# Kernel tuning notes

Measured on AMD Instinct MI355X. Metric: run time of the kernel, lower is better.

## Reference

```python
import jax, jax.numpy as jnp
import numpy as np

EPS = 1e-12  # torch F.normalize eps


def setup_inputs() -> dict:
    key = jax.random.key(0)
    k1, k2, k3 = jax.random.split(key, 3)
    b, c, n, h, w = 8, 64, 8, 64, 64
    dims = 32
    x = jax.random.normal(k1, (b, c, n, h, w), dtype=jnp.float32)
    # 1x1 conv kernels collapse to [out_ch, in_ch] matrices
    w_q = jax.random.normal(k2, (dims, c), dtype=jnp.float32) * (1.0 / np.sqrt(c))
    w_kv = jax.random.normal(k3, (2 * dims, c), dtype=jnp.float32) * (1.0 / np.sqrt(c))
    return {"x": x, "w_q": w_q, "w_kv": w_kv}


def _l2norm(t, axis):
    nrm = jnp.sqrt(jnp.sum(t * t, axis=axis, keepdims=True))
    return t / jnp.maximum(nrm, EPS)


def reference(x, w_q, w_kv):
    b, c, n, h, w = x.shape
    d = w_q.shape[0]
    # spa_q: 1x1 stride-1 conv == channel GEMM -> [b, d, n, h, w]
    q = jnp.einsum('bcnhw,dc->bdnhw', x, w_q)
    x_s = x[:, :, :, ::2, ::2]                       # [b, c, n, h2, w2]
    kv = jnp.einsum('bcnhw,ec->benhw', x_s, w_kv)    # [b, 2d, n, h2, w2]
    k, v = kv[:, :d], kv[:, d:]
    h2, w2 = k.shape[-2], k.shape[-1]
    # unfold_q: b (h w) (d n)
    uq = q.transpose(0, 3, 4, 1, 2).reshape(b, h * w, d * n)
    # unfold_k: b (d n) (h2 w2)
    uk = k.reshape(b, d * n, h2 * w2)
    # unfold_v: b (h2 w2) (d n)
    uv = v.transpose(0, 3, 4, 1, 2).reshape(b, h2 * w2, d * n)
    uq = _l2norm(uq, axis=-1)
    uk = _l2norm(uk, axis=-2)
    att = jax.nn.softmax(jnp.einsum('bqf,bfk->bqk', uq, uk), axis=-1)
    out = jnp.einsum('bqk,bkf->bqf', att, uv)        # [b, h*w, d*n]
    # b (h w) (d n) -> b d n h w
    return out.reshape(b, h, w, d, n).transpose(0, 3, 4, 1, 2)
```

## Files before the change

### kernel.cpp

```cpp
#include <hip/hip_runtime.h>


typedef __attribute__((ext_vector_type(8))) short short8;
typedef __attribute__((ext_vector_type(4))) float floatx4;
typedef __attribute__((ext_vector_type(2))) unsigned uintx2;

__device__ __forceinline__ short f2bf(float f) {
    unsigned u = __builtin_bit_cast(unsigned, f);
    u += 0x7fffu + ((u >> 16) & 1u);
    return (short)(u >> 16);
}

__device__ __forceinline__ unsigned cvtpk_bf16(float lo, float hi) {
    unsigned r;
    asm("v_cvt_pk_bf16_f32 %0, %1, %2" : "=v"(r) : "v"(lo), "v"(hi));
    return r;
}

__global__ __launch_bounds__(256) void proj(const float* __restrict__ x,
                                            const float* __restrict__ wq,
                                            const float* __restrict__ wkv,
                                            short* __restrict__ qraw,
                                            short* __restrict__ kraw,
                                            short* __restrict__ vraw) {
    int b = blockIdx.x >> 6, y = blockIdx.x & 63;
    int t = threadIdx.x;
    int n = t >> 5, dg = (t >> 3) & 3, xc = t & 7;
    bool kv = (y & 1) == 0;
    int y2 = y >> 1;

    __shared__ __align__(16) float wq_s[64 * 32];
    __shared__ __align__(16) float wkv_s[64 * 64];
    __shared__ __align__(16) float xs[128 * 36];
    __shared__ __align__(16) short k_lds[16 * 264];
    __shared__ __align__(16) short v_lds[256 * 16];
    __shared__ float red[32 * 33];
    __shared__ float nrm[32];
    short* q_lds = (short*)xs;

    for (int i = t; i < 2048; i += 256) { int d = i >> 6, c = i & 63; wq_s[c * 32 + d] = wq[i]; }
    for (int i = t; i < 4096; i += 256) { int e = i >> 6, c = i & 63; wkv_s[c * 64 + e] = wkv[i]; }
    const float* xb = x + (size_t)b * 2097152 + y * 64;

    for (int xh = 0; xh < 2; ++xh) {
        float qa[8][4], ka[8][2], va[8][2];
#pragma unroll
        for (int j = 0; j < 8; ++j) {
            qa[j][0] = qa[j][1] = qa[j][2] = qa[j][3] = 0.f;
            ka[j][0] = ka[j][1] = 0.f; va[j][0] = va[j][1] = 0.f;
        }
        for (int cc = 0; cc < 4; ++cc) {
            __syncthreads();
#pragma unroll
            for (int it = 0; it < 4; ++it) {
                int i = it * 256 + t, cn = i >> 3, e = i & 7;
                float4 v = *(const float4*)(xb + (size_t)(cc * 16 + (cn >> 3)) * 32768 + (cn & 7) * 4096 + xh * 32 + e * 4);
                *(float4*)(xs + cn * 36 + e * 4) = v;
            }
            __syncthreads();
            for (int c = 0; c < 16; ++c) {
                float4 xv = *(const float4*)(xs + (c * 8 + n) * 36 + xc * 4);
                float xw[4] = {xv.x, xv.y, xv.z, xv.w};
                int cg = cc * 16 + c;
                float4 wqa = *(const float4*)(wq_s + cg * 32 + dg * 8);
                float4 wqb = *(const float4*)(wq_s + cg * 32 + dg * 8 + 4);
                float wj[8] = {wqa.x, wqa.y, wqa.z, wqa.w, wqb.x, wqb.y, wqb.z, wqb.w};
#pragma unroll
                for (int j = 0; j < 8; ++j)
#pragma unroll
                    for (int i2 = 0; i2 < 4; ++i2) qa[j][i2] += wj[j] * xw[i2];
                if (kv) {
                    float4 wka = *(const float4*)(wkv_s + cg * 64 + dg * 8);
                    float4 wkb = *(const float4*)(wkv_s + cg * 64 + dg * 8 + 4);
                    float4 wva = *(const float4*)(wkv_s + cg * 64 + 32 + dg * 8);
                    float4 wvb = *(const float4*)(wkv_s + cg * 64 + 32 + dg * 8 + 4);
                    float wk[8] = {wka.x, wka.y, wka.z, wka.w, wkb.x, wkb.y, wkb.z, wkb.w};
                    float wv2[8] = {wva.x, wva.y, wva.z, wva.w, wvb.x, wvb.y, wvb.z, wvb.w};
#pragma unroll
                    for (int j = 0; j < 8; ++j) {
                        ka[j][0] += wk[j] * xw[0]; ka[j][1] += wk[j] * xw[2];
                        va[j][0] += wv2[j] * xw[0]; va[j][1] += wv2[j] * xw[2];
                    }
                }
            }
        }
        __syncthreads();
#pragma unroll
        for (int i2 = 0; i2 < 4; ++i2) {
            float s = 0.f;
#pragma unroll
            for (int j = 0; j < 8; ++j) s += qa[j][i2] * qa[j][i2];
            red[(xc * 4 + i2) * 33 + n * 4 + dg] = s;
        }
        __syncthreads();
        if (t < 32) {
            float s = 0.f;
            for (int k = 0; k < 32; ++k) s += red[t * 33 + k];
            nrm[t] = 1.f / fmaxf(sqrtf(s), 1e-12f);
        }
        __syncthreads();
#pragma unroll
        for (int i2 = 0; i2 < 4; ++i2) {
            float sc = nrm[xc * 4 + i2];
#pragma unroll
            for (int j = 0; j < 8; ++j)
                q_lds[(xc * 4 + i2) * 264 + (dg * 8 + j) * 8 + n] = f2bf(qa[j][i2] * sc);
        }
        __syncthreads();
        {
            size_t qg = ((size_t)b * 4096 + y * 64 + xh * 32) * 256;
#pragma unroll
            for (int it = 0; it < 4; ++it) {
                int r = it * 8 + (t >> 5), sg = t & 31;
                *(uint4*)(qraw + qg + (size_t)r * 256 + sg * 8) = *(const uint4*)(q_lds + r * 264 + sg * 8);
            }
        }
        if (kv) {
            __syncthreads();
#pragma unroll
            for (int ii = 0; ii < 2; ++ii) {
                float s = 0.f;
#pragma unroll
                for (int j = 0; j < 8; ++j) s += ka[j][ii] * ka[j][ii];
                red[(xc * 2 + ii) * 33 + n * 4 + dg] = s;
            }
            __syncthreads();
            if (t < 16) {
                float s = 0.f;
                for (int k = 0; k < 32; ++k) s += red[t * 33 + k];
                nrm[t] = 1.f / fmaxf(sqrtf(s), 1e-12f);
            }
            __syncthreads();
#pragma unroll
            for (int ii = 0; ii < 2; ++ii) {
                float sc = nrm[xc * 2 + ii];
#pragma unroll
                for (int j = 0; j < 8; ++j) {
                    int f = (dg * 8 + j) * 8 + n;
                    k_lds[(xc * 2 + ii) * 264 + f] = f2bf(ka[j][ii] * sc);
                    v_lds[f * 16 + xc * 2 + ii] = f2bf(va[j][ii]);
                }
            }
            __syncthreads();
            size_t kg = ((size_t)b * 1024 + y2 * 32 + xh * 16) * 256;
#pragma unroll
            for (int it = 0; it < 2; ++it) {
                int r = it * 8 + (t >> 5), sg = t & 31;
                *(uint4*)(kraw + kg + (size_t)r * 256 + sg * 8) = *(const uint4*)(k_lds + r * 264 + sg * 8);
            }
            size_t vg = (size_t)b * 262144 + (size_t)y2 * 32 + xh * 16;
#pragma unroll
            for (int it = 0; it < 2; ++it) {
                int idx = it * 256 + t, f = idx >> 1, hh = idx & 1;
                *(uint4*)(vraw + vg + (size_t)f * 1024 + hh * 8) = *(const uint4*)(v_lds + f * 16 + hh * 8);
            }
        }
    }
}

__global__ __launch_bounds__(512, 2) void attn(const short* __restrict__ qraw,
                                               const short* __restrict__ kraw,
                                               const short* __restrict__ vraw,
                                               float* __restrict__ out) {
    int b = blockIdx.x >> 5, qt = blockIdx.x & 31;
    int t = threadIdx.x, wv = t >> 6, lane = t & 63, l16 = lane & 15, quad = lane >> 4;

    __shared__ __align__(16) short k_s[2][32 * 264];
    __shared__ __align__(16) short v_s[2][256 * 40];
    __shared__ __align__(16) short p_s[2][128 * 40];
    __shared__ float dsum[2][128];

    int kt = wv & 1, pp = wv >> 1;
    int fh = wv & 3, ph = wv >> 2;

    short8 qf[2][8];
    const short* qb = qraw + ((size_t)b * 4096 + qt * 128 + pp * 32) * 256;
#pragma unroll
    for (int pt = 0; pt < 2; ++pt)
#pragma unroll
        for (int fs = 0; fs < 8; ++fs)
            qf[pt][fs] = *(const short8*)(qb + (pt * 16 + l16) * 256 + fs * 32 + quad * 8);

    floatx4 acc[4][4];
#pragma unroll
    for (int i = 0; i < 4; ++i)
#pragma unroll
        for (int j = 0; j < 4; ++j) acc[i][j] = (floatx4){0.f, 0.f, 0.f, 0.f};
    float dacc0 = 0.f, dacc1 = 0.f;

    int krow = t >> 4, kseg = t & 15;
    int vrow = t >> 1, vhalf = t & 1;
    int sk = (kseg >> 2) & 1, sv = (t >> 4) & 1;
    const short* kbase = kraw + ((size_t)b * 1024 + krow) * 256 + kseg * 16;
    const short* vbase = vraw + ((size_t)b * 256 + vrow) * 1024 + vhalf * 16;

    short8 kst[2], vst[2];
#pragma unroll
    for (int j = 0; j < 2; ++j) {
        kst[j] = *(const short8*)(kbase + j * 8);
        vst[j] = *(const short8*)(vbase + j * 8);
    }
#pragma unroll
    for (int j = 0; j < 2; ++j) {
        *(short8*)(k_s[0] + krow * 264 + kseg * 16 + (j ^ sk) * 8) = kst[j];
        *(short8*)(v_s[0] + vrow * 40 + vhalf * 16 + (j ^ sv) * 8) = vst[j];
    }
#pragma unroll
    for (int j = 0; j < 2; ++j) {
        kst[j] = *(const short8*)(kbase + 8192 + j * 8);
        vst[j] = *(const short8*)(vbase + 32 + j * 8);
    }
    __syncthreads();

    int s2 = (l16 >> 3) & 1;
    for (int kc = 0; kc < 32; ++kc) {
        int cur = kc & 1, nxt = cur ^ 1;
        floatx4 cc0 = (floatx4){0.f, 0.f, 0.f, 0.f};
        floatx4 cc1 = (floatx4){0.f, 0.f, 0.f, 0.f};
        const short* krd = k_s[cur] + (kt * 16 + l16) * 264;
        __builtin_amdgcn_s_setprio(1);
#pragma unroll
        for (int fs = 0; fs < 8; ++fs) {
            short8 a = *(const short8*)(krd + fs * 32 + (quad ^ ((fs >> 1) & 1)) * 8);
            cc0 = __builtin_amdgcn_mfma_f32_16x16x32_bf16(a, qf[0][fs], cc0, 0, 0, 0);
            cc1 = __builtin_amdgcn_mfma_f32_16x16x32_bf16(a, qf[1][fs], cc1, 0, 0, 0);
        }
        __builtin_amdgcn_s_setprio(0);
        {
            float e0 = __expf(cc0[0]), e1 = __expf(cc0[1]);
            float e2 = __expf(cc0[2]), e3 = __expf(cc0[3]);
            dacc0 += (e0 + e1) + (e2 + e3);
            uintx2 w0; w0[0] = cvtpk_bf16(e0, e1); w0[1] = cvtpk_bf16(e2, e3);
            *(uintx2*)(p_s[cur] + (pp * 32 + l16) * 40 + kt * 16 + quad * 4) = w0;
            float f0 = __expf(cc1[0]), f1 = __expf(cc1[1]);
            float f2 = __expf(cc1[2]), f3 = __expf(cc1[3]);
            dacc1 += (f0 + f1) + (f2 + f3);
            uintx2 w1; w1[0] = cvtpk_bf16(f0, f1); w1[1] = cvtpk_bf16(f2, f3);
            *(uintx2*)(p_s[cur] + (pp * 32 + 16 + l16) * 40 + kt * 16 + quad * 4) = w1;
        }
        __syncthreads();

        if (kc < 31) {
#pragma unroll
            for (int j = 0; j < 2; ++j) {
                *(short8*)(k_s[nxt] + krow * 264 + kseg * 16 + (j ^ sk) * 8) = kst[j];
                *(short8*)(v_s[nxt] + vrow * 40 + vhalf * 16 + (j ^ sv) * 8) = vst[j];
            }
        }
        short8 av[4];
#pragma unroll
        for (int fl = 0; fl < 4; ++fl)
            av[fl] = *(const short8*)(v_s[cur] + (fh * 64 + fl * 16 + l16) * 40 + (quad ^ s2) * 8);
        __builtin_amdgcn_s_setprio(1);
#pragma unroll
        for (int p2 = 0; p2 < 4; ++p2) {
            short8 bq = *(const short8*)(p_s[cur] + (ph * 64 + p2 * 16 + l16) * 40 + quad * 8);
#pragma unroll
            for (int fl = 0; fl < 4; ++fl)
                acc[p2][fl] = __builtin_amdgcn_mfma_f32_16x16x32_bf16(av[fl], bq, acc[p2][fl], 0, 0, 0);
        }
        __builtin_amdgcn_s_setprio(0);
        if (kc < 30) {
            int koff = (kc + 2) * 8192, voff = (kc + 2) * 32;
#pragma unroll
            for (int j = 0; j < 2; ++j) {
                kst[j] = *(const short8*)(kbase + koff + j * 8);
                vst[j] = *(const short8*)(vbase + voff + j * 8);
            }
        }
        __syncthreads();
    }
    dacc0 += __shfl_xor(dacc0, 16); dacc0 += __shfl_xor(dacc0, 32);
    dacc1 += __shfl_xor(dacc1, 16); dacc1 += __shfl_xor(dacc1, 32);
    if (quad == 0) {
        dsum[kt][pp * 32 + l16] = dacc0;
        dsum[kt][pp * 32 + 16 + l16] = dacc1;
    }
    __syncthreads();
    float* ob = out + (size_t)b * 1048576 + qt * 128;
#pragma unroll
    for (int p2 = 0; p2 < 4; ++p2) {
        int pcol = ph * 64 + p2 * 16 + l16;
        float inv = 1.f / (dsum[0][pcol] + dsum[1][pcol]);
#pragma unroll
        for (int fl = 0; fl < 4; ++fl) {
            int f0 = fh * 64 + fl * 16 + quad * 4;
#pragma unroll
            for (int r = 0; r < 4; ++r)
                ob[(size_t)(f0 + r) * 4096 + pcol] = acc[p2][fl][r] * inv;
        }
    }
}

extern "C" void kernel_launch(void* const* d_in, const int* in_sizes, int n_in,
                              void* d_out, int out_size, void* d_ws, size_t ws_size,
                              hipStream_t stream) {
    (void)in_sizes; (void)n_in; (void)out_size; (void)ws_size;
    const float* x   = (const float*)d_in[0];
    const float* wqp = (const float*)d_in[1];
    const float* wkv = (const float*)d_in[2];
    float* out = (float*)d_out;

    char* ws = (char*)d_ws;
    short* qraw = (short*)ws;
    short* kraw = (short*)(ws + 16777216);
    short* vraw = (short*)(ws + 16777216 + 4194304);

    proj<<<512, 256, 0, stream>>>(x, wqp, wkv, qraw, kraw, vraw);
    attn<<<256, 512, 0, stream>>>(qraw, kraw, vraw, out);
}
```

Baseline: 184.0 us.

## Process both x-halves in parallel with 512-thread proj blocks and swizzled LDS stores

```diff
diff --git a/kernel.cpp b/kernel.cpp
--- a/kernel.cpp
+++ b/kernel.cpp
@@ -17,80 +17,114 @@
     return r;
 }
 
-__global__ __launch_bounds__(256) void proj(const float* __restrict__ x,
-                                            const float* __restrict__ wq,
-                                            const float* __restrict__ wkv,
-                                            short* __restrict__ qraw,
-                                            short* __restrict__ kraw,
-                                            short* __restrict__ vraw) {
+__global__ __launch_bounds__(512, 4) void proj(const float* __restrict__ x,
+                                               const float* __restrict__ wq,
+                                               const float* __restrict__ wkv,
+                                               short* __restrict__ qraw,
+                                               short* __restrict__ kraw,
+                                               short* __restrict__ vraw) {
     int b = blockIdx.x >> 6, y = blockIdx.x & 63;
     int t = threadIdx.x;
-    int n = t >> 5, dg = (t >> 3) & 3, xc = t & 7;
+    int th = t & 255, xh = t >> 8;
+    int n = th >> 5, dg = (th >> 3) & 3, xc = th & 7;
     bool kv = (y & 1) == 0;
     int y2 = y >> 1;
 
     __shared__ __align__(16) float wq_s[64 * 32];
     __shared__ __align__(16) float wkv_s[64 * 64];
-    __shared__ __align__(16) float xs[128 * 36];
-    __shared__ __align__(16) short k_lds[16 * 264];
-    __shared__ __align__(16) short v_lds[256 * 16];
-    __shared__ float red[32 * 33];
-    __shared__ float nrm[32];
-    short* q_lds = (short*)xs;
-
-    for (int i = t; i < 2048; i += 256) { int d = i >> 6, c = i & 63; wq_s[c * 32 + d] = wq[i]; }
-    for (int i = t; i < 4096; i += 256) { int e = i >> 6, c = i & 63; wkv_s[c * 64 + e] = wkv[i]; }
+    __shared__ __align__(16) char region[37376];
+    __shared__ float red[64 * 33];
+    __shared__ float nrm[64];
+    float* xs    = (float*)region;
+    short* q_lds = (short*)region;
+    short* k_lds = (short*)region;
+    short* v_lds = (short*)(region + 16896);
+
+    for (int i = t; i < 2048; i += 512) { int d = i >> 6, c = i & 63; wq_s[c * 32 + d] = wq[i]; }
+    for (int i = t; i < 4096; i += 512) { int e = i >> 6, c = i & 63; wkv_s[c * 64 + e] = wkv[i]; }
     const float* xb = x + (size_t)b * 2097152 + y * 64;
 
-    for (int xh = 0; xh < 2; ++xh) {
-        float qa[8][4], ka[8][2], va[8][2];
-#pragma unroll
-        for (int j = 0; j < 8; ++j) {
-            qa[j][0] = qa[j][1] = qa[j][2] = qa[j][3] = 0.f;
-            ka[j][0] = ka[j][1] = 0.f; va[j][0] = va[j][1] = 0.f;
-        }
-        for (int cc = 0; cc < 4; ++cc) {
-            __syncthreads();
-#pragma unroll
-            for (int it = 0; it < 4; ++it) {
-                int i = it * 256 + t, cn = i >> 3, e = i & 7;
-                float4 v = *(const float4*)(xb + (size_t)(cc * 16 + (cn >> 3)) * 32768 + (cn & 7) * 4096 + xh * 32 + e * 4);
-                *(float4*)(xs + cn * 36 + e * 4) = v;
-            }
-            __syncthreads();
-            for (int c = 0; c < 16; ++c) {
-                float4 xv = *(const float4*)(xs + (c * 8 + n) * 36 + xc * 4);
-                float xw[4] = {xv.x, xv.y, xv.z, xv.w};
-                int cg = cc * 16 + c;
-                float4 wqa = *(const float4*)(wq_s + cg * 32 + dg * 8);
-                float4 wqb = *(const float4*)(wq_s + cg * 32 + dg * 8 + 4);
-                float wj[8] = {wqa.x, wqa.y, wqa.z, wqa.w, wqb.x, wqb.y, wqb.z, wqb.w};
-#pragma unroll
-                for (int j = 0; j < 8; ++j)
-#pragma unroll
-                    for (int i2 = 0; i2 < 4; ++i2) qa[j][i2] += wj[j] * xw[i2];
-                if (kv) {
-                    float4 wka = *(const float4*)(wkv_s + cg * 64 + dg * 8);
-                    float4 wkb = *(const float4*)(wkv_s + cg * 64 + dg * 8 + 4);
-                    float4 wva = *(const float4*)(wkv_s + cg * 64 + 32 + dg * 8);
-                    float4 wvb = *(const float4*)(wkv_s + cg * 64 + 32 + dg * 8 + 4);
-                    float wk[8] = {wka.x, wka.y, wka.z, wka.w, wkb.x, wkb.y, wkb.z, wkb.w};
-                    float wv2[8] = {wva.x, wva.y, wva.z, wva.w, wvb.x, wvb.y, wvb.z, wvb.w};
-#pragma unroll
-                    for (int j = 0; j < 8; ++j) {
-                        ka[j][0] += wk[j] * xw[0]; ka[j][1] += wk[j] * xw[2];
-                        va[j][0] += wv2[j] * xw[0]; va[j][1] += wv2[j] * xw[2];
-                    }
+    float qa[8][4], ka[8][2], va[8][2];
+#pragma unroll
+    for (int j = 0; j < 8; ++j) {
+        qa[j][0] = qa[j][1] = qa[j][2] = qa[j][3] = 0.f;
+        ka[j][0] = ka[j][1] = 0.f; va[j][0] = va[j][1] = 0.f;
+    }
+    for (int cc = 0; cc < 4; ++cc) {
+        __syncthreads();
+#pragma unroll
+        for (int it = 0; it < 4; ++it) {
+            int i = it * 512 + t, cn = i >> 4, e = i & 15;
+            float4 v = *(const float4*)(xb + (size_t)(cc * 16 + (cn >> 3)) * 32768 + (cn & 7) * 4096 + e * 4);
+            *(float4*)(xs + cn * 72 + e * 4) = v;
+        }
+        __syncthreads();
+        for (int c = 0; c < 16; ++c) {
+            float4 xv = *(const float4*)(xs + (c * 8 + n) * 72 + xh * 32 + xc * 4);
+            float xw[4] = {xv.x, xv.y, xv.z, xv.w};
+            int cg = cc * 16 + c;
+            float4 wqa = *(const float4*)(wq_s + cg * 32 + dg * 8);
+            float4 wqb = *(const float4*)(wq_s + cg * 32 + dg * 8 + 4);
+            float wj[8] = {wqa.x, wqa.y, wqa.z, wqa.w, wqb.x, wqb.y, wqb.z, wqb.w};
+#pragma unroll
+            for (int j = 0; j < 8; ++j)
+#pragma unroll
+                for (int i2 = 0; i2 < 4; ++i2) qa[j][i2] += wj[j] * xw[i2];
+            if (kv) {
+                float4 wka = *(const float4*)(wkv_s + cg * 64 + dg * 8);
+                float4 wkb = *(const float4*)(wkv_s + cg * 64 + dg * 8 + 4);
+                float4 wva = *(const float4*)(wkv_s + cg * 64 + 32 + dg * 8);
+                float4 wvb = *(const float4*)(wkv_s + cg * 64 + 32 + dg * 8 + 4);
+                float wk[8] = {wka.x, wka.y, wka.z, wka.w, wkb.x, wkb.y, wkb.z, wkb.w};
+                float wv2[8] = {wva.x, wva.y, wva.z, wva.w, wvb.x, wvb.y, wvb.z, wvb.w};
+#pragma unroll
+                for (int j = 0; j < 8; ++j) {
+                    ka[j][0] += wk[j] * xw[0]; ka[j][1] += wk[j] * xw[2];
+                    va[j][0] += wv2[j] * xw[0]; va[j][1] += wv2[j] * xw[2];
                 }
             }
         }
-        __syncthreads();
-#pragma unroll
-        for (int i2 = 0; i2 < 4; ++i2) {
+    }
+#pragma unroll
+    for (int i2 = 0; i2 < 4; ++i2) {
+        float s = 0.f;
+#pragma unroll
+        for (int j = 0; j < 8; ++j) s += qa[j][i2] * qa[j][i2];
+        red[(xh * 32 + xc * 4 + i2) * 33 + n * 4 + dg] = s;
+    }
+    __syncthreads();
+    if (t < 64) {
+        float s = 0.f;
+        for (int k = 0; k < 32; ++k) s += red[t * 33 + k];
+        nrm[t] = 1.f / fmaxf(sqrtf(s), 1e-12f);
+    }
+    __syncthreads();
+#pragma unroll
+    for (int i2 = 0; i2 < 4; ++i2) {
+        int row = xh * 32 + xc * 4 + i2;
+        float sc = nrm[row];
+#pragma unroll
+        for (int j = 0; j < 8; ++j)
+            q_lds[row * 264 + (dg * 8 + (j ^ dg)) * 8 + n] = f2bf(qa[j][i2] * sc);
+    }
+    __syncthreads();
+    {
+        size_t qg = ((size_t)b * 4096 + y * 64) * 256;
+#pragma unroll
+        for (int it = 0; it < 4; ++it) {
+            int idx = it * 512 + t, r = idx >> 5, sg = idx & 31;
+            *(uint4*)(qraw + qg + (size_t)r * 256 + sg * 8) =
+                *(const uint4*)(q_lds + r * 264 + (sg ^ ((sg >> 3) & 3)) * 8);
+        }
+    }
+    if (kv) {
+        __syncthreads();
+#pragma unroll
+        for (int ii = 0; ii < 2; ++ii) {
             float s = 0.f;
 #pragma unroll
-            for (int j = 0; j < 8; ++j) s += qa[j][i2] * qa[j][i2];
-            red[(xc * 4 + i2) * 33 + n * 4 + dg] = s;
+            for (int j = 0; j < 8; ++j) s += ka[j][ii] * ka[j][ii];
+            red[(xh * 16 + xc * 2 + ii) * 33 + n * 4 + dg] = s;
         }
         __syncthreads();
         if (t < 32) {
@@ -100,60 +134,28 @@
         }
         __syncthreads();
 #pragma unroll
-        for (int i2 = 0; i2 < 4; ++i2) {
-            float sc = nrm[xc * 4 + i2];
-#pragma unroll
-            for (int j = 0; j < 8; ++j)
-                q_lds[(xc * 4 + i2) * 264 + (dg * 8 + j) * 8 + n] = f2bf(qa[j][i2] * sc);
-        }
-        __syncthreads();
-        {
-            size_t qg = ((size_t)b * 4096 + y * 64 + xh * 32) * 256;
-#pragma unroll
-            for (int it = 0; it < 4; ++it) {
-                int r = it * 8 + (t >> 5), sg = t & 31;
-                *(uint4*)(qraw + qg + (size_t)r * 256 + sg * 8) = *(const uint4*)(q_lds + r * 264 + sg * 8);
+        for (int ii = 0; ii < 2; ++ii) {
+            int row = xh * 16 + xc * 2 + ii;
+            float sc = nrm[row];
+#pragma unroll
+            for (int j = 0; j < 8; ++j) {
+                k_lds[row * 264 + (dg * 8 + (j ^ dg)) * 8 + n] = f2bf(ka[j][ii] * sc);
+                v_lds[(dg * 64 + j * 8 + n) * 40 + row] = f2bf(va[j][ii]);
             }
         }
-        if (kv) {
-            __syncthreads();
-#pragma unroll
-            for (int ii = 0; ii < 2; ++ii) {
-                float s = 0.f;
-#pragma unroll
-                for (int j = 0; j < 8; ++j) s += ka[j][ii] * ka[j][ii];
-                red[(xc * 2 + ii) * 33 + n * 4 + dg] = s;
-            }
-            __syncthreads();
-            if (t < 16) {
-                float s = 0.f;
-                for (int k = 0; k < 32; ++k) s += red[t * 33 + k];
-                nrm[t] = 1.f / fmaxf(sqrtf(s), 1e-12f);
-            }
-            __syncthreads();
-#pragma unroll
-            for (int ii = 0; ii < 2; ++ii) {
-                float sc = nrm[xc * 2 + ii];
-#pragma unroll
-                for (int j = 0; j < 8; ++j) {
-                    int f = (dg * 8 + j) * 8 + n;
-                    k_lds[(xc * 2 + ii) * 264 + f] = f2bf(ka[j][ii] * sc);
-                    v_lds[f * 16 + xc * 2 + ii] = f2bf(va[j][ii]);
-                }
-            }
-            __syncthreads();
-            size_t kg = ((size_t)b * 1024 + y2 * 32 + xh * 16) * 256;
-#pragma unroll
-            for (int it = 0; it < 2; ++it) {
-                int r = it * 8 + (t >> 5), sg = t & 31;
-                *(uint4*)(kraw + kg + (size_t)r * 256 + sg * 8) = *(const uint4*)(k_lds + r * 264 + sg * 8);
-            }
-            size_t vg = (size_t)b * 262144 + (size_t)y2 * 32 + xh * 16;
-#pragma unroll
-            for (int it = 0; it < 2; ++it) {
-                int idx = it * 256 + t, f = idx >> 1, hh = idx & 1;
-                *(uint4*)(vraw + vg + (size_t)f * 1024 + hh * 8) = *(const uint4*)(v_lds + f * 16 + hh * 8);
-            }
+        __syncthreads();
+        size_t kg = ((size_t)b * 1024 + y2 * 32) * 256;
+#pragma unroll
+        for (int it = 0; it < 2; ++it) {
+            int idx = it * 512 + t, r = idx >> 5, sg = idx & 31;
+            *(uint4*)(kraw + kg + (size_t)r * 256 + sg * 8) =
+                *(const uint4*)(k_lds + r * 264 + (sg ^ ((sg >> 3) & 3)) * 8);
+        }
+        size_t vg = (size_t)b * 262144 + (size_t)y2 * 32;
+#pragma unroll
+        for (int it = 0; it < 2; ++it) {
+            int idx = it * 512 + t, f = idx >> 2, qq = idx & 3;
+            *(uint4*)(vraw + vg + (size_t)f * 1024 + qq * 8) = *(const uint4*)(v_lds + f * 40 + qq * 8);
         }
     }
 }
@@ -306,6 +308,6 @@
     short* kraw = (short*)(ws + 16777216);
     short* vraw = (short*)(ws + 16777216 + 4194304);
 
-    proj<<<512, 256, 0, stream>>>(x, wqp, wkv, qraw, kraw, vraw);
+    proj<<<512, 512, 0, stream>>>(x, wqp, wkv, qraw, kraw, vraw);
     attn<<<256, 512, 0, stream>>>(qraw, kraw, vraw, out);
 }
```

New measurement: 479.7 us. 2.61x slower.
